# Performance work log

Measured on AMD Instinct MI355X. Metric: run time of the kernel, lower is better.

The kernel has to match this reference:

```python
import jax, jax.numpy as jnp
import numpy as np

N_NODES = 10000
N_EDGES = 320000
D = 128
H = 4
C = 128
L = 2
NEG_SLOPE = 0.2
LN_EPS = 1e-5


def setup_inputs() -> dict:
    key = jax.random.key(0)
    ks = jax.random.split(key, 8)
    x = jax.random.normal(ks[0], (N_NODES, D), dtype=jnp.float32)
    edge_index = jax.random.randint(ks[1], (2, N_EDGES), 0, N_NODES, dtype=jnp.int64)
    # weights scaled ~Glorot to keep attention logits in a sane range
    Wl = jax.random.normal(ks[2], (L, D, H * C), dtype=jnp.float32) * 0.1
    Wr = jax.random.normal(ks[3], (L, D, H * C), dtype=jnp.float32) * 0.1
    att = jax.random.normal(ks[4], (L, H, C), dtype=jnp.float32) * 0.1
    return {
        "x": x,
        "edge_index": edge_index,
        "Wl": Wl,
        "bl": jnp.zeros((L, H * C), jnp.float32),
        "Wr": Wr,
        "br": jnp.zeros((L, H * C), jnp.float32),
        "att": att,
        "bias": jnp.zeros((L, D), jnp.float32),
        "ln_g": jnp.ones((L, D), jnp.float32),
        "ln_b": jnp.zeros((L, D), jnp.float32),
    }


def _gatv2_layer(x, src, dst, Wl, bl, Wr, br, att, b):
    """GATv2Conv (concat=False -> head mean), messages src->dst, softmax over dst."""
    n = x.shape[0]
    xl = (x @ Wl + bl).reshape(n, H, C)  # source transform
    xr = (x @ Wr + br).reshape(n, H, C)  # target transform
    s = jax.nn.leaky_relu(xl[src] + xr[dst], NEG_SLOPE)  # [E, H, C]
    e = jnp.einsum("ehc,hc->eh", s, att)  # attention logits [E, H]
    m = jax.ops.segment_max(e, dst, num_segments=n)  # stable softmax per dst segment
    ex = jnp.exp(e - m[dst])
    denom = jax.ops.segment_sum(ex, dst, num_segments=n)
    alpha = ex / denom[dst]  # [E, H]
    out = jax.ops.segment_sum(alpha[:, :, None] * xl[src], dst, num_segments=n)  # [N, H, C]
    return out.mean(axis=1) + b  # concat=False -> mean over heads, then bias


def _layer_norm(h, g, b):
    mu = h.mean(-1, keepdims=True)
    var = ((h - mu) ** 2).mean(-1, keepdims=True)
    return (h - mu) * jax.lax.rsqrt(var + LN_EPS) * g + b


def reference(x, edge_index, Wl, bl, Wr, br, att, bias, ln_g, ln_b):
    n = x.shape[0]
    loop = jnp.arange(n, dtype=edge_index.dtype)
    src = jnp.concatenate([edge_index[0], loop])  # add self-loops (PyG default)
    dst = jnp.concatenate([edge_index[1], loop])
    for i in range(L):
        h = _gatv2_layer(x, src, dst, Wl[i], bl[i], Wr[i], br[i], att[i], bias[i])
        x = h + x  # residual
        x = jax.nn.relu(_layer_norm(x, ln_g[i], ln_b[i]))
    return x
```

## Files before the change

kernel.cpp:

```cpp
#include <hip/hip_runtime.h>
#include <math.h>

#define N_NODES 10000
#define N_EDGES 320000
#define E_TOT   (N_EDGES + N_NODES)
#define NEG 0.2f
#define CAP 96

typedef short bf16x8 __attribute__((ext_vector_type(8)));
typedef float f32x4 __attribute__((ext_vector_type(4)));
typedef float f32x2 __attribute__((ext_vector_type(2)));

static __device__ __forceinline__ float4 ld4g(const float* p) { return *(const float4*)p; }

static __device__ __forceinline__ uint4 ldg4(const unsigned short* p, unsigned byteoff) {
    return *(const uint4*)((const char*)p + byteoff);
}
static __device__ __forceinline__ int ldgi(const int* p, int e) { return p[e]; }

static __device__ __forceinline__ unsigned short f2b(float f) {
    unsigned u;
    __builtin_memcpy(&u, &f, 4);
    unsigned r = (u + 0x7fffu + ((u >> 16) & 1u)) >> 16;
    return (unsigned short)r;
}
static __device__ __forceinline__ f32x2 unpk(unsigned d) {
    f32x2 r;
    r.x = __uint_as_float(d << 16);
    r.y = __uint_as_float(d & 0xffff0000u);
    return r;
}

template <int CTRL>
static __device__ __forceinline__ float dpp_add_step(float x) {
    int y = __builtin_amdgcn_update_dpp(0, __float_as_int(x), CTRL, 0xf, 0xf, true);
    return x + __int_as_float(y);
}
static __device__ __forceinline__ float row_sum16(float x) {
    x = dpp_add_step<0x121>(x);
    x = dpp_add_step<0x122>(x);
    x = dpp_add_step<0x124>(x);
    x = dpp_add_step<0x128>(x);
    return x;
}

static __device__ __forceinline__ void comp_full(
    uint4 u,
    const f32x2* __restrict__ xr2, const f32x2* __restrict__ at2,
    f32x2* __restrict__ acc2, float* __restrict__ dsum) {
    const f32x2 neg2 = {NEG, NEG};
    const unsigned* w = (const unsigned*)&u;
    f32x2 F[4];
#pragma unroll
    for (int q = 0; q < 4; ++q) F[q] = unpk(w[q]);
    f32x2 qq = {0.f, 0.f};
#pragma unroll
    for (int q = 0; q < 4; ++q) {
        f32x2 s = F[q] + xr2[q];
        s = __builtin_elementwise_max(s, s * neg2);
        qq = __builtin_elementwise_fma(s, at2[q], qq);
    }
    float ev = __expf(row_sum16(qq.x + qq.y));
    *dsum += ev;
    f32x2 W = {ev, ev};
#pragma unroll
    for (int q = 0; q < 4; ++q)
        acc2[q] = __builtin_elementwise_fma(F[q], W, acc2[q]);
}

static __device__ __forceinline__ void comp_mask(
    uint4 u, bool valid,
    const f32x2* __restrict__ xr2, const f32x2* __restrict__ at2,
    f32x2* __restrict__ acc2, float* __restrict__ dsum) {
    const f32x2 neg2 = {NEG, NEG};
    const unsigned* w = (const unsigned*)&u;
    f32x2 F[4];
#pragma unroll
    for (int q = 0; q < 4; ++q) F[q] = unpk(w[q]);
    f32x2 qq = {0.f, 0.f};
#pragma unroll
    for (int q = 0; q < 4; ++q) {
        f32x2 s = F[q] + xr2[q];
        s = __builtin_elementwise_max(s, s * neg2);
        qq = __builtin_elementwise_fma(s, at2[q], qq);
    }
    float ev = __expf(row_sum16(qq.x + qq.y));
    ev = valid ? ev : 0.f;
    *dsum += ev;
    f32x2 W = {ev, ev};
#pragma unroll
    for (int q = 0; q < 4; ++q)
        acc2[q] = __builtin_elementwise_fma(F[q], W, acc2[q]);
}

__global__ __launch_bounds__(256) void prep_fused_kernel(
    const float* __restrict__ x,
    const float* __restrict__ Wl, const float* __restrict__ Wr,
    unsigned short* __restrict__ xb, unsigned short* __restrict__ WT,
    int* __restrict__ deg) {
    int tid = threadIdx.x, bid = blockIdx.x;
    __shared__ float tbuf[32][33];

    for (int i = bid * 256 + tid; i < N_NODES; i += 256 * 256) deg[i] = 0;

    int l = bid >> 7;
    int rest = bid & 127;
    int ky = rest >> 5, nx = rest & 31;
    int n0 = nx * 32, k0 = ky * 32;
    const float* S = ((n0 < 512) ? Wl : Wr) + (size_t)l * 65536;
    int nn0 = n0 & 511;
    int tx = tid & 31, ty = tid >> 5;
#pragma unroll
    for (int it = 0; it < 4; ++it) {
        int k = k0 + ty + it * 8;
        tbuf[ty + it * 8][tx] = S[(size_t)k * 512 + nn0 + tx];
    }
    __syncthreads();
    unsigned short* dstp = WT + (size_t)l * 1024 * 128;
#pragma unroll
    for (int it = 0; it < 4; ++it) {
        int n = n0 + ty + it * 8;
        int k = k0 + tx;
        dstp[(size_t)n * 128 + k] = f2b(tbuf[tx][ty + it * 8]);
    }
    for (int i = bid * 256 + tid; i < N_NODES * 32; i += 256 * 256) {
        float4 v = ld4g(x + 4 * i);
        ushort4 o = make_ushort4(f2b(v.x), f2b(v.y), f2b(v.z), f2b(v.w));
        *(ushort4*)(xb + 4 * i) = o;
    }
}

template <int DO_FILL>
__global__ __launch_bounds__(256) void gemm_mfma_kernel(const unsigned short* __restrict__ A,
                                                        const unsigned short* __restrict__ Bt,
                                                        const float* __restrict__ bl,
                                                        const float* __restrict__ br,
                                                        unsigned short* __restrict__ xlh,
                                                        unsigned short* __restrict__ xrh,
                                                        const int* __restrict__ ei,
                                                        int* __restrict__ deg,
                                                        int* __restrict__ csr_src) {
    __shared__ unsigned short Bs[2][128][72];
    int tid = threadIdx.x;
    int wave = tid >> 6, lane = tid & 63;
    int l15 = lane & 15, quad = lane >> 4;
    int row0 = blockIdx.y * 128, col0 = blockIdx.x * 128;
    const float* bias = (col0 < 512) ? (bl + col0) : (br + col0 - 512);

    bf16x8 st[8];
    {
        const unsigned short* src = Bt + (size_t)(col0 + (tid >> 1)) * 128 + (size_t)(tid & 1) * 64;
#pragma unroll
        for (int j = 0; j < 8; ++j) st[j] = *(const bf16x8*)(src + j * 8);
    }

    bf16x8 af[2][2][2];
#pragma unroll
    for (int mi = 0; mi < 2; ++mi) {
        int row = row0 + wave * 32 + mi * 16 + l15;
        int rr = (row < N_NODES) ? row : 0;
        const unsigned short* ap = A + ((size_t)rr << 7);
#pragma unroll
        for (int kc = 0; kc < 2; ++kc)
#pragma unroll
            for (int kq = 0; kq < 2; ++kq)
                af[mi][kc][kq] = *(const bf16x8*)(ap + kc * 64 + kq * 32 + quad * 8);
    }

#pragma unroll
    for (int j = 0; j < 8; ++j) *(bf16x8*)&Bs[tid & 1][tid >> 1][j * 8] = st[j];
    __syncthreads();

    f32x4 acc[2][8];
#pragma unroll
    for (int mi = 0; mi < 2; ++mi)
#pragma unroll
        for (int ni = 0; ni < 8; ++ni)
#pragma unroll
            for (int r = 0; r < 4; ++r) acc[mi][ni][r] = 0.f;

#pragma unroll
    for (int kc = 0; kc < 2; ++kc) {
#pragma unroll
        for (int kq = 0; kq < 2; ++kq) {
            bf16x8 bfr[8];
#pragma unroll
            for (int ni = 0; ni < 8; ++ni)
                bfr[ni] = *(const bf16x8*)&Bs[kc][ni * 16 + l15][kq * 32 + quad * 8];
#pragma unroll
            for (int mi = 0; mi < 2; ++mi)
#pragma unroll
                for (int ni = 0; ni < 8; ++ni)
                    acc[mi][ni] = __builtin_amdgcn_mfma_f32_16x16x32_bf16(af[mi][kc][kq], bfr[ni], acc[mi][ni], 0, 0, 0);
        }
    }

    float bv[8];
#pragma unroll
    for (int ni = 0; ni < 8; ++ni) bv[ni] = bias[ni * 16 + l15];

    int h = (col0 >> 7) & 3;
    unsigned short* dstb = ((col0 < 512) ? xlh : xrh) + (((size_t)h * N_NODES) << 7);

#pragma unroll
    for (int mi = 0; mi < 2; ++mi) {
#pragma unroll
        for (int r = 0; r < 4; ++r) {
            int grow = row0 + wave * 32 + mi * 16 + quad * 4 + r;
            if (grow >= N_NODES) continue;
#pragma unroll
            for (int ni = 0; ni < 8; ++ni)
                dstb[((size_t)grow << 7) + ni * 16 + l15] = f2b(acc[mi][ni][r] + bv[ni]);
        }
    }

    if (DO_FILL) {
        bool is64 = ((ei[1] | ei[3] | ei[5] | ei[7]) == 0);
        int nthreads = gridDim.x * gridDim.y * 256;
        int gid = (blockIdx.y * gridDim.x + blockIdx.x) * 256 + tid;
        for (int i = gid; i < E_TOT; i += nthreads) {
            int src, dst;
            if (i < N_EDGES) {
                if (is64) { const long long* e = (const long long*)ei; src = (int)e[i]; dst = (int)e[N_EDGES + i]; }
                else { src = ei[i]; dst = ei[N_EDGES + i]; }
            } else {
                src = dst = i - N_EDGES;
            }
            int pos = atomicAdd(&deg[dst], 1);
            if (pos < CAP) csr_src[dst * CAP + pos] = src;
        }
    }
}

__global__ __launch_bounds__(256) void attn_kernel(
    const unsigned short* __restrict__ xlh,
    const unsigned short* __restrict__ xrh,
    const int* __restrict__ deg, const int* __restrict__ csr_src,
    const float* __restrict__ att,
    float* __restrict__ hpart) {
    int tid = threadIdx.x;
    unsigned bid = blockIdx.x;
    int w = tid >> 6, lane = tid & 63;
    int head = __builtin_amdgcn_readfirstlane((int)((bid & 7u) >> 1));
    int slot = (int)((bid >> 3) * 2 + (bid & 1u));
    int e = lane >> 4, g = lane & 15;
    unsigned gboff = (unsigned)(g << 4);

    const unsigned short* XL = xlh + (((size_t)head * N_NODES) << 7);
    const unsigned short* XR = xrh + (((size_t)head * N_NODES) << 7);
    float* HP = hpart + (((size_t)head * N_NODES) << 7);

    f32x2 at2[4];
    {
        const float* ap = att + head * 128 + g * 8;
        float4 a = ld4g(ap);
        float4 b = ld4g(ap + 4);
        at2[0].x = a.x; at2[0].y = a.y; at2[1].x = a.z; at2[1].y = a.w;
        at2[2].x = b.x; at2[2].y = b.y; at2[3].x = b.z; at2[3].y = b.w;
    }

    for (int dst0 = slot * 4 + w; dst0 < N_NODES; dst0 += 2048) {
        int dst = __builtin_amdgcn_readfirstlane(dst0);

        f32x2 xr2[4];
        {
            uint4 u = *(const uint4*)(XR + ((size_t)dst << 7) + g * 8);
            xr2[0] = unpk(u.x); xr2[1] = unpk(u.y); xr2[2] = unpk(u.z); xr2[3] = unpk(u.w);
        }

        int len = deg[dst];
        if (len > CAP) len = CAP;
        const int* cp = csr_src + dst * CAP;
        int full = len >> 2, rem = len & 3;

        float d = 0.f;
        f32x2 acc2[4] = {{0.f, 0.f}, {0.f, 0.f}, {0.f, 0.f}, {0.f, 0.f}};

        if (full) {
            int idx = ldgi(cp, e);
            uint4 uc = ldg4(XL, ((unsigned)idx << 8) + gboff);
            for (int r = 0; r + 1 < full; ++r) {
                int i1 = ldgi(cp + 4 * (r + 1), e);
                uint4 un = ldg4(XL, ((unsigned)i1 << 8) + gboff);
                comp_full(uc, xr2, at2, acc2, &d);
                uc = un;
            }
            comp_full(uc, xr2, at2, acc2, &d);
        }
        if (rem) {
            int raw = ldgi(cp + 4 * full, e);
            int idx = (e < rem) ? raw : 0;
            uint4 u = ldg4(XL, ((unsigned)idx << 8) + gboff);
            comp_mask(u, e < rem, xr2, at2, acc2, &d);
        }

        float t[8];
#pragma unroll
        for (int q = 0; q < 4; ++q) { t[2 * q] = acc2[q].x; t[2 * q + 1] = acc2[q].y; }
#pragma unroll
        for (int j = 0; j < 8; ++j) {
            t[j] += __shfl_xor(t[j], 16, 64);
            t[j] += __shfl_xor(t[j], 32, 64);
        }
        float ds = d;
        ds += __shfl_xor(ds, 16, 64);
        ds += __shfl_xor(ds, 32, 64);
        float inv = 1.f / ds;
#pragma unroll
        for (int j = 0; j < 8; ++j) t[j] *= inv;

        if (lane < 16) {
            float* op = HP + ((size_t)dst << 7) + g * 8;
            *(float4*)op = make_float4(t[0], t[1], t[2], t[3]);
            *(float4*)(op + 4) = make_float4(t[4], t[5], t[6], t[7]);
        }
    }
}

__global__ __launch_bounds__(256) void combine_kernel(
    const float* __restrict__ hpart, const float* __restrict__ x_in,
    const float* __restrict__ bias, const float* __restrict__ ln_g,
    const float* __restrict__ ln_b, float* __restrict__ x_out,
    unsigned short* __restrict__ xb_out) {
    int wv = (blockIdx.x * blockDim.x + threadIdx.x) >> 6;
    if (wv >= N_NODES) return;
    int lane = threadIdx.x & 63;
    int dst = __builtin_amdgcn_readfirstlane(wv);
    int c = lane * 2;
    const float* hp = hpart + ((size_t)dst << 7) + c;
    const size_t hs = ((size_t)N_NODES) << 7;
    f32x2 h0 = *(const f32x2*)(hp);
    f32x2 h1 = *(const f32x2*)(hp + hs);
    f32x2 h2 = *(const f32x2*)(hp + 2 * hs);
    f32x2 h3 = *(const f32x2*)(hp + 3 * hs);
    f32x2 bi = *(const f32x2*)(bias + c);
    f32x2 xi = *(const f32x2*)(x_in + ((size_t)dst << 7) + c);
    f32x2 hc = ((h0 + h1) + (h2 + h3)) * 0.25f + bi + xi;
    float sm = hc.x + hc.y;
    float sq = hc.x * hc.x + hc.y * hc.y;
    sm = row_sum16(sm); sm += __shfl_xor(sm, 16, 64); sm += __shfl_xor(sm, 32, 64);
    sq = row_sum16(sq); sq += __shfl_xor(sq, 16, 64); sq += __shfl_xor(sq, 32, 64);
    float mu = sm * (1.f / 128.f);
    float var = sq * (1.f / 128.f) - mu * mu;
    float rs = rsqrtf(var + 1e-5f);
    f32x2 gg = *(const f32x2*)(ln_g + c);
    f32x2 bb = *(const f32x2*)(ln_b + c);
    float y0 = fmaxf((hc.x - mu) * rs * gg.x + bb.x, 0.f);
    float y1 = fmaxf((hc.y - mu) * rs * gg.y + bb.y, 0.f);
    f32x2 y = {y0, y1};
    *(f32x2*)(x_out + ((size_t)dst << 7) + c) = y;
    if (xb_out) {
        unsigned pk = ((unsigned)f2b(y0)) | (((unsigned)f2b(y1)) << 16);
        *(unsigned*)(xb_out + ((size_t)dst << 7) + c) = pk;
    }
}

extern "C" void kernel_launch(void* const* d_in, const int* in_sizes, int n_in,
                              void* d_out, int out_size, void* d_ws, size_t ws_size,
                              hipStream_t stream) {
    const float* x    = (const float*)d_in[0];
    const int*   ei   = (const int*)d_in[1];
    const float* Wl   = (const float*)d_in[2];
    const float* bl   = (const float*)d_in[3];
    const float* Wr   = (const float*)d_in[4];
    const float* br   = (const float*)d_in[5];
    const float* att  = (const float*)d_in[6];
    const float* bias = (const float*)d_in[7];
    const float* lng  = (const float*)d_in[8];
    const float* lnb  = (const float*)d_in[9];
    float* out = (float*)d_out;

    char* ws = (char*)d_ws;
    unsigned short* xlh = (unsigned short*)ws; ws += (size_t)4 * N_NODES * 128 * 2;
    unsigned short* xrh = (unsigned short*)ws; ws += (size_t)4 * N_NODES * 128 * 2;
    float* hpart = (float*)ws;          ws += (size_t)4 * N_NODES * 128 * 4;
    float* xbuf  = (float*)ws;          ws += (size_t)N_NODES * 128 * 4;
    unsigned short* xb = (unsigned short*)ws; ws += (size_t)N_NODES * 128 * 2;
    unsigned short* WT = (unsigned short*)ws; ws += (size_t)2 * 1024 * 128 * 2;
    int* deg     = (int*)ws;            ws += (size_t)N_NODES * 4;
    int* csr_src = (int*)ws;            ws += (size_t)N_NODES * CAP * 4;

    prep_fused_kernel<<<256, 256, 0, stream>>>(x, Wl, Wr, xb, WT, deg);

    for (int l = 0; l < 2; ++l) {
        const float* xin = (l == 0) ? x : xbuf;
        float* xout = (l == 0) ? xbuf : out;
        unsigned short* xbo = (l == 0) ? xb : (unsigned short*)nullptr;
        if (l == 0)
            gemm_mfma_kernel<1><<<dim3(8, 79), 256, 0, stream>>>(
                xb, WT, bl, br, xlh, xrh, ei, deg, csr_src);
        else
            gemm_mfma_kernel<0><<<dim3(8, 79), 256, 0, stream>>>(
                xb, WT + (size_t)1024 * 128, bl + 512, br + 512, xlh, xrh, ei, deg, csr_src);
        attn_kernel<<<2048, 256, 0, stream>>>(
            xlh, xrh, deg, csr_src, att + (size_t)l * 512, hpart);
        combine_kernel<<<2500, 256, 0, stream>>>(
            hpart, xin, bias + (size_t)l * 128,
            lng + (size_t)l * 128, lnb + (size_t)l * 128, xout, xbo);
    }
}
```

Measured before the change: 210.5 us.

## Fuse attention aggregation with head-mean, residual and LayerNorm via shared memory

Merges the attention kernel and the combine kernel into one kernel. Each block handles 4 destination nodes, with each wave computing one head. Per-head results go to LDS instead of a global hpart buffer, then each wave does the head mean, residual and LayerNorm for one node. This removes a launch and the global write and read of the 4xNx128 float partials. In exchange it changes the work mapping: head-major blocks no longer sweep nodes in a stride pattern, and every block now waits at a barrier behind its slowest wave.

```diff
diff --git a/kernel.cpp b/kernel.cpp
--- a/kernel.cpp
+++ b/kernel.cpp
@@ -232,23 +232,23 @@
     }
 }
 
-__global__ __launch_bounds__(256) void attn_kernel(
+__global__ __launch_bounds__(256) void attn_combine_kernel(
     const unsigned short* __restrict__ xlh,
     const unsigned short* __restrict__ xrh,
     const int* __restrict__ deg, const int* __restrict__ csr_src,
     const float* __restrict__ att,
-    float* __restrict__ hpart) {
+    const float* __restrict__ x_in, const float* __restrict__ bias,
+    const float* __restrict__ ln_g, const float* __restrict__ ln_b,
+    float* __restrict__ x_out, unsigned short* __restrict__ xb_out) {
+    __shared__ float hbuf[4][4][128];
     int tid = threadIdx.x;
-    unsigned bid = blockIdx.x;
     int w = tid >> 6, lane = tid & 63;
-    int head = __builtin_amdgcn_readfirstlane((int)((bid & 7u) >> 1));
-    int slot = (int)((bid >> 3) * 2 + (bid & 1u));
+    int head = __builtin_amdgcn_readfirstlane(w);
     int e = lane >> 4, g = lane & 15;
     unsigned gboff = (unsigned)(g << 4);
 
     const unsigned short* XL = xlh + (((size_t)head * N_NODES) << 7);
     const unsigned short* XR = xrh + (((size_t)head * N_NODES) << 7);
-    float* HP = hpart + (((size_t)head * N_NODES) << 7);
 
     f32x2 at2[4];
     {
@@ -259,8 +259,11 @@
         at2[2].x = b.x; at2[2].y = b.y; at2[3].x = b.z; at2[3].y = b.w;
     }
 
-    for (int dst0 = slot * 4 + w; dst0 < N_NODES; dst0 += 2048) {
-        int dst = __builtin_amdgcn_readfirstlane(dst0);
+    int base = blockIdx.x * 4;
+
+#pragma unroll 1
+    for (int i = 0; i < 4; ++i) {
+        int dst = __builtin_amdgcn_readfirstlane(base + i);
 
         f32x2 xr2[4];
         {
@@ -310,48 +313,41 @@
         for (int j = 0; j < 8; ++j) t[j] *= inv;
 
         if (lane < 16) {
-            float* op = HP + ((size_t)dst << 7) + g * 8;
+            float* op = &hbuf[i][head][g * 8];
             *(float4*)op = make_float4(t[0], t[1], t[2], t[3]);
             *(float4*)(op + 4) = make_float4(t[4], t[5], t[6], t[7]);
         }
     }
-}
-
-__global__ __launch_bounds__(256) void combine_kernel(
-    const float* __restrict__ hpart, const float* __restrict__ x_in,
-    const float* __restrict__ bias, const float* __restrict__ ln_g,
-    const float* __restrict__ ln_b, float* __restrict__ x_out,
-    unsigned short* __restrict__ xb_out) {
-    int wv = (blockIdx.x * blockDim.x + threadIdx.x) >> 6;
-    if (wv >= N_NODES) return;
-    int lane = threadIdx.x & 63;
-    int dst = __builtin_amdgcn_readfirstlane(wv);
-    int c = lane * 2;
-    const float* hp = hpart + ((size_t)dst << 7) + c;
-    const size_t hs = ((size_t)N_NODES) << 7;
-    f32x2 h0 = *(const f32x2*)(hp);
-    f32x2 h1 = *(const f32x2*)(hp + hs);
-    f32x2 h2 = *(const f32x2*)(hp + 2 * hs);
-    f32x2 h3 = *(const f32x2*)(hp + 3 * hs);
-    f32x2 bi = *(const f32x2*)(bias + c);
-    f32x2 xi = *(const f32x2*)(x_in + ((size_t)dst << 7) + c);
-    f32x2 hc = ((h0 + h1) + (h2 + h3)) * 0.25f + bi + xi;
-    float sm = hc.x + hc.y;
-    float sq = hc.x * hc.x + hc.y * hc.y;
-    sm = row_sum16(sm); sm += __shfl_xor(sm, 16, 64); sm += __shfl_xor(sm, 32, 64);
-    sq = row_sum16(sq); sq += __shfl_xor(sq, 16, 64); sq += __shfl_xor(sq, 32, 64);
-    float mu = sm * (1.f / 128.f);
-    float var = sq * (1.f / 128.f) - mu * mu;
-    float rs = rsqrtf(var + 1e-5f);
-    f32x2 gg = *(const f32x2*)(ln_g + c);
-    f32x2 bb = *(const f32x2*)(ln_b + c);
-    float y0 = fmaxf((hc.x - mu) * rs * gg.x + bb.x, 0.f);
-    float y1 = fmaxf((hc.y - mu) * rs * gg.y + bb.y, 0.f);
-    f32x2 y = {y0, y1};
-    *(f32x2*)(x_out + ((size_t)dst << 7) + c) = y;
-    if (xb_out) {
-        unsigned pk = ((unsigned)f2b(y0)) | (((unsigned)f2b(y1)) << 16);
-        *(unsigned*)(xb_out + ((size_t)dst << 7) + c) = pk;
+
+    __syncthreads();
+
+    {
+        int dst = __builtin_amdgcn_readfirstlane(base + w);
+        int c = lane * 2;
+        f32x2 h0 = *(const f32x2*)&hbuf[w][0][c];
+        f32x2 h1 = *(const f32x2*)&hbuf[w][1][c];
+        f32x2 h2 = *(const f32x2*)&hbuf[w][2][c];
+        f32x2 h3 = *(const f32x2*)&hbuf[w][3][c];
+        f32x2 bi = *(const f32x2*)(bias + c);
+        f32x2 xi = *(const f32x2*)(x_in + ((size_t)dst << 7) + c);
+        f32x2 hc = ((h0 + h1) + (h2 + h3)) * 0.25f + bi + xi;
+        float sm = hc.x + hc.y;
+        float sq = hc.x * hc.x + hc.y * hc.y;
+        sm = row_sum16(sm); sm += __shfl_xor(sm, 16, 64); sm += __shfl_xor(sm, 32, 64);
+        sq = row_sum16(sq); sq += __shfl_xor(sq, 16, 64); sq += __shfl_xor(sq, 32, 64);
+        float mu = sm * (1.f / 128.f);
+        float var = sq * (1.f / 128.f) - mu * mu;
+        float rs = rsqrtf(var + 1e-5f);
+        f32x2 gg = *(const f32x2*)(ln_g + c);
+        f32x2 bb = *(const f32x2*)(ln_b + c);
+        float y0 = fmaxf((hc.x - mu) * rs * gg.x + bb.x, 0.f);
+        float y1 = fmaxf((hc.y - mu) * rs * gg.y + bb.y, 0.f);
+        f32x2 y = {y0, y1};
+        *(f32x2*)(x_out + ((size_t)dst << 7) + c) = y;
+        if (xb_out) {
+            unsigned pk = ((unsigned)f2b(y0)) | (((unsigned)f2b(y1)) << 16);
+            *(unsigned*)(xb_out + ((size_t)dst << 7) + c) = pk;
+        }
     }
 }
 
@@ -373,7 +369,6 @@
     char* ws = (char*)d_ws;
     unsigned short* xlh = (unsigned short*)ws; ws += (size_t)4 * N_NODES * 128 * 2;
     unsigned short* xrh = (unsigned short*)ws; ws += (size_t)4 * N_NODES * 128 * 2;
-    float* hpart = (float*)ws;          ws += (size_t)4 * N_NODES * 128 * 4;
     float* xbuf  = (float*)ws;          ws += (size_t)N_NODES * 128 * 4;
     unsigned short* xb = (unsigned short*)ws; ws += (size_t)N_NODES * 128 * 2;
     unsigned short* WT = (unsigned short*)ws; ws += (size_t)2 * 1024 * 128 * 2;
@@ -392,10 +387,9 @@
         else
             gemm_mfma_kernel<0><<<dim3(8, 79), 256, 0, stream>>>(
                 xb, WT + (size_t)1024 * 128, bl + 512, br + 512, xlh, xrh, ei, deg, csr_src);
-        attn_kernel<<<2048, 256, 0, stream>>>(
-            xlh, xrh, deg, csr_src, att + (size_t)l * 512, hpart);
-        combine_kernel<<<2500, 256, 0, stream>>>(
-            hpart, xin, bias + (size_t)l * 128,
+        attn_combine_kernel<<<2500, 256, 0, stream>>>(
+            xlh, xrh, deg, csr_src, att + (size_t)l * 512,
+            xin, bias + (size_t)l * 128,
             lng + (size_t)l * 128, lnb + (size_t)l * 128, xout, xbo);
     }
 }
```

Measured after the change: 216.2 us. +2.7%, slower.

## Split CSR fill into its own kernel and halve GEMM row tile

Applied to the files above, without the earlier changes.

Moves the edge-to-CSR atomic fill out of the layer-0 GEMM into a dedicated 640-block kernel launched after prep. The GEMM now handles 64 rows per block (one 16-row MFMA tile per wave) on a 157-row grid, doubling block count for better CU occupancy on the small 10000-row problem. This removes the tail where GEMM blocks also ran the atomic scatter loop. In exchange it adds an extra launch and halves reuse of the B tile loaded into shared memory per block.

```diff
diff --git a/kernel.cpp b/kernel.cpp
--- a/kernel.cpp
+++ b/kernel.cpp
@@ -130,21 +130,35 @@
     }
 }
 
-template <int DO_FILL>
+__global__ __launch_bounds__(256) void csr_fill_kernel(
+    const int* __restrict__ ei, int* __restrict__ deg, int* __restrict__ csr_src) {
+    bool is64 = ((ei[1] | ei[3] | ei[5] | ei[7]) == 0);
+    int nthreads = gridDim.x * 256;
+    int gid = blockIdx.x * 256 + threadIdx.x;
+    for (int i = gid; i < E_TOT; i += nthreads) {
+        int src, dst;
+        if (i < N_EDGES) {
+            if (is64) { const long long* e = (const long long*)ei; src = (int)e[i]; dst = (int)e[N_EDGES + i]; }
+            else { src = ei[i]; dst = ei[N_EDGES + i]; }
+        } else {
+            src = dst = i - N_EDGES;
+        }
+        int pos = atomicAdd(&deg[dst], 1);
+        if (pos < CAP) csr_src[dst * CAP + pos] = src;
+    }
+}
+
 __global__ __launch_bounds__(256) void gemm_mfma_kernel(const unsigned short* __restrict__ A,
                                                         const unsigned short* __restrict__ Bt,
                                                         const float* __restrict__ bl,
                                                         const float* __restrict__ br,
                                                         unsigned short* __restrict__ xlh,
-                                                        unsigned short* __restrict__ xrh,
-                                                        const int* __restrict__ ei,
-                                                        int* __restrict__ deg,
-                                                        int* __restrict__ csr_src) {
+                                                        unsigned short* __restrict__ xrh) {
     __shared__ unsigned short Bs[2][128][72];
     int tid = threadIdx.x;
     int wave = tid >> 6, lane = tid & 63;
     int l15 = lane & 15, quad = lane >> 4;
-    int row0 = blockIdx.y * 128, col0 = blockIdx.x * 128;
+    int row0 = blockIdx.y * 64, col0 = blockIdx.x * 128;
     const float* bias = (col0 < 512) ? (bl + col0) : (br + col0 - 512);
 
     bf16x8 st[8];
@@ -154,30 +168,27 @@
         for (int j = 0; j < 8; ++j) st[j] = *(const bf16x8*)(src + j * 8);
     }
 
-    bf16x8 af[2][2][2];
-#pragma unroll
-    for (int mi = 0; mi < 2; ++mi) {
-        int row = row0 + wave * 32 + mi * 16 + l15;
+    bf16x8 af[2][2];
+    {
+        int row = row0 + wave * 16 + l15;
         int rr = (row < N_NODES) ? row : 0;
         const unsigned short* ap = A + ((size_t)rr << 7);
 #pragma unroll
         for (int kc = 0; kc < 2; ++kc)
 #pragma unroll
             for (int kq = 0; kq < 2; ++kq)
-                af[mi][kc][kq] = *(const bf16x8*)(ap + kc * 64 + kq * 32 + quad * 8);
+                af[kc][kq] = *(const bf16x8*)(ap + kc * 64 + kq * 32 + quad * 8);
     }
 
 #pragma unroll
     for (int j = 0; j < 8; ++j) *(bf16x8*)&Bs[tid & 1][tid >> 1][j * 8] = st[j];
     __syncthreads();
 
-    f32x4 acc[2][8];
-#pragma unroll
-    for (int mi = 0; mi < 2; ++mi)
-#pragma unroll
-        for (int ni = 0; ni < 8; ++ni)
-#pragma unroll
-            for (int r = 0; r < 4; ++r) acc[mi][ni][r] = 0.f;
+    f32x4 acc[8];
+#pragma unroll
+    for (int ni = 0; ni < 8; ++ni)
+#pragma unroll
+        for (int r = 0; r < 4; ++r) acc[ni][r] = 0.f;
 
 #pragma unroll
     for (int kc = 0; kc < 2; ++kc) {
@@ -188,10 +199,8 @@
             for (int ni = 0; ni < 8; ++ni)
                 bfr[ni] = *(const bf16x8*)&Bs[kc][ni * 16 + l15][kq * 32 + quad * 8];
 #pragma unroll
-            for (int mi = 0; mi < 2; ++mi)
-#pragma unroll
-                for (int ni = 0; ni < 8; ++ni)
-                    acc[mi][ni] = __builtin_amdgcn_mfma_f32_16x16x32_bf16(af[mi][kc][kq], bfr[ni], acc[mi][ni], 0, 0, 0);
+            for (int ni = 0; ni < 8; ++ni)
+                acc[ni] = __builtin_amdgcn_mfma_f32_16x16x32_bf16(af[kc][kq], bfr[ni], acc[ni], 0, 0, 0);
         }
     }
 
@@ -203,32 +212,12 @@
     unsigned short* dstb = ((col0 < 512) ? xlh : xrh) + (((size_t)h * N_NODES) << 7);
 
 #pragma unroll
-    for (int mi = 0; mi < 2; ++mi) {
-#pragma unroll
-        for (int r = 0; r < 4; ++r) {
-            int grow = row0 + wave * 32 + mi * 16 + quad * 4 + r;
-            if (grow >= N_NODES) continue;
-#pragma unroll
-            for (int ni = 0; ni < 8; ++ni)
-                dstb[((size_t)grow << 7) + ni * 16 + l15] = f2b(acc[mi][ni][r] + bv[ni]);
-        }
-    }
-
-    if (DO_FILL) {
-        bool is64 = ((ei[1] | ei[3] | ei[5] | ei[7]) == 0);
-        int nthreads = gridDim.x * gridDim.y * 256;
-        int gid = (blockIdx.y * gridDim.x + blockIdx.x) * 256 + tid;
-        for (int i = gid; i < E_TOT; i += nthreads) {
-            int src, dst;
-            if (i < N_EDGES) {
-                if (is64) { const long long* e = (const long long*)ei; src = (int)e[i]; dst = (int)e[N_EDGES + i]; }
-                else { src = ei[i]; dst = ei[N_EDGES + i]; }
-            } else {
-                src = dst = i - N_EDGES;
-            }
-            int pos = atomicAdd(&deg[dst], 1);
-            if (pos < CAP) csr_src[dst * CAP + pos] = src;
-        }
+    for (int r = 0; r < 4; ++r) {
+        int grow = row0 + wave * 16 + quad * 4 + r;
+        if (grow >= N_NODES) continue;
+#pragma unroll
+        for (int ni = 0; ni < 8; ++ni)
+            dstb[((size_t)grow << 7) + ni * 16 + l15] = f2b(acc[ni][r] + bv[ni]);
     }
 }
 
@@ -381,17 +370,15 @@
     int* csr_src = (int*)ws;            ws += (size_t)N_NODES * CAP * 4;
 
     prep_fused_kernel<<<256, 256, 0, stream>>>(x, Wl, Wr, xb, WT, deg);
+    csr_fill_kernel<<<640, 256, 0, stream>>>(ei, deg, csr_src);
 
     for (int l = 0; l < 2; ++l) {
         const float* xin = (l == 0) ? x : xbuf;
         float* xout = (l == 0) ? xbuf : out;
         unsigned short* xbo = (l == 0) ? xb : (unsigned short*)nullptr;
-        if (l == 0)
-            gemm_mfma_kernel<1><<<dim3(8, 79), 256, 0, stream>>>(
-                xb, WT, bl, br, xlh, xrh, ei, deg, csr_src);
-        else
-            gemm_mfma_kernel<0><<<dim3(8, 79), 256, 0, stream>>>(
-                xb, WT + (size_t)1024 * 128, bl + 512, br + 512, xlh, xrh, ei, deg, csr_src);
+        gemm_mfma_kernel<<<dim3(8, 157), 256, 0, stream>>>(
+            xb, WT + (size_t)l * 1024 * 128,
+            bl + (size_t)l * 512, br + (size_t)l * 512, xlh, xrh);
         attn_kernel<<<2048, 256, 0, stream>>>(
             xlh, xrh, deg, csr_src, att + (size_t)l * 512, hpart);
         combine_kernel<<<2500, 256, 0, stream>>>(
```

Measured after the change: 221.8 us. +5.4%, slower.
